# Performance work log

Hardware: AMD Instinct MI355X
Metric: run time of the kernel (lower is better)

Reference implementation:

```python
import jax, jax.numpy as jnp
import numpy as np

V, E, H, LM, LC = 50257, 512, 1024, 128, 256


def gru_cell(x, h, Wih, Whh, bih, bhh):
    # PyTorch nn.GRU cell, gate order (r, z, n)
    gi = x @ Wih.T + bih
    gh = h @ Whh.T + bhh
    i_r, i_z, i_n = jnp.split(gi, 3, -1)
    h_r, h_z, h_n = jnp.split(gh, 3, -1)
    r = jax.nn.sigmoid(i_r + h_r)
    z = jax.nn.sigmoid(i_z + h_z)
    n = jnp.tanh(i_n + r * h_n)
    return (1.0 - z) * n + z * h


def setup_inputs() -> dict:
    key = jax.random.key(0)
    ks = jax.random.split(key, 18)
    f = lambda k, sh: jax.random.normal(k, sh, jnp.float32) * 0.02
    return {
        "motion": jax.random.randint(ks[0], (1, LM), 0, V),
        "target_output": jax.random.randint(ks[1], (1, LC), 0, V),
        "enc_emb": f(ks[2], (V, E)),
        "enc_Wih": f(ks[3], (3 * H, E)),
        "enc_Whh": f(ks[4], (3 * H, H)),
        "enc_bih": f(ks[5], (3 * H,)),
        "enc_bhh": f(ks[6], (3 * H,)),
        "dec_emb": f(ks[7], (V, H)),
        "dec_Wih": f(ks[8], (3 * H, H)),
        "dec_Whh": f(ks[9], (3 * H, H)),
        "dec_bih": f(ks[10], (3 * H,)),
        "dec_bhh": f(ks[11], (3 * H,)),
        "attn_W": f(ks[12], (LM, 2 * H)),
        "attn_b": f(ks[13], (LM,)),
        "comb_W": f(ks[14], (H, 2 * H)),
        "comb_b": f(ks[15], (H,)),
        "out_W": f(ks[16], (V, H)),
        "out_b": f(ks[17], (V,)),
    }


def reference(motion, target_output, enc_emb, enc_Wih, enc_Whh, enc_bih, enc_bhh,
              dec_emb, dec_Wih, dec_Whh, dec_bih, dec_bhh,
              attn_W, attn_b, comb_W, comb_b, out_W, out_b):
    # ----- encode: per-step GRU over motion tokens (batch is hard-coded 1) -----
    toks = motion[0]  # [LM]

    def enc_step(h, t):
        h2 = gru_cell(enc_emb[t], h, enc_Wih, enc_Whh, enc_bih, enc_bhh)
        return h2, h2

    h0 = jnp.zeros((H,), jnp.float32)
    enc_h, enc_outs = jax.lax.scan(enc_step, h0, toks)  # enc_outs: [LM, H]

    # ----- decode with teacher forcing -----
    # original: decoder_input = SOS at idx 0, then target[idx-1] set at end of
    # step idx => step idx+1 consumes target[idx-1]; step 1 consumes target[-1].
    tgt = target_output[0]  # [LC]
    dec_in = jnp.concatenate([jnp.zeros((1,), tgt.dtype), tgt[-1:], tgt[:-2]])  # [LC]

    def dec_step(h, t):
        emb = dec_emb[t]  # [H] (dropout is identity at inference)
        attn_w = jax.nn.softmax(jnp.concatenate([emb, h]) @ attn_W.T + attn_b)  # [LM]
        ctx = attn_w @ enc_outs  # [H]
        x = jnp.concatenate([emb, ctx]) @ comb_W.T + comb_b  # [H] (no relu in source)
        h2 = gru_cell(x, h, dec_Wih, dec_Whh, dec_bih, dec_bhh)
        logp = jax.nn.log_softmax(h2 @ out_W.T + out_b)  # [V]
        return h2, logp

    _, logps = jax.lax.scan(dec_step, enc_h, dec_in)  # [LC, V]
    return logps[None]  # [1, LC, V] (permute(1,0,2) with batch=1)
```

## Files before the change

### kernel.cpp

```cpp
#include <hip/hip_runtime.h>

#define V_ 50257
#define E_ 512
#define H_ 1024
#define LM_ 128
#define LC_ 256
#define NBLK 256
#define ROWS 12
#define AREP 16

typedef __attribute__((ext_vector_type(8))) short short8;
typedef __attribute__((ext_vector_type(4))) float f32x4;
typedef unsigned long long u64;

__device__ __forceinline__ unsigned short f2bf(float x) {
  union { float f; unsigned u; } v; v.f = x;
  unsigned r = v.u + 0x7fffu + ((v.u >> 16) & 1u);
  return (unsigned short)(r >> 16);
}
__device__ __forceinline__ float bflo(unsigned u) { union { unsigned u; float f; } v; v.u = u << 16; return v.f; }
__device__ __forceinline__ float bfhi(unsigned u) { union { unsigned u; float f; } v; v.u = u & 0xffff0000u; return v.f; }

__device__ __forceinline__ int grow4(int s, int i0) {
  return (s < 4) ? (i0 + s) : (s < 8) ? (1024 + i0 + (s - 4)) : (2048 + i0 + (s - 8));
}

__device__ __forceinline__ void st_u32(unsigned* p, unsigned v) {
  __hip_atomic_store(p, v, __ATOMIC_RELAXED, __HIP_MEMORY_SCOPE_AGENT);
}
__device__ __forceinline__ void st_u64(u64* p, u64 v) {
  __hip_atomic_store(p, v, __ATOMIC_RELAXED, __HIP_MEMORY_SCOPE_AGENT);
}
__device__ __forceinline__ u64 ld_u64(const u64* p) {
  return __hip_atomic_load(p, __ATOMIC_RELAXED, __HIP_MEMORY_SCOPE_AGENT);
}
__device__ __forceinline__ unsigned ld_u32(const unsigned* p) {
  return __hip_atomic_load(p, __ATOMIC_RELAXED, __HIP_MEMORY_SCOPE_AGENT);
}
__device__ __forceinline__ float ld_f32(const float* p) {
  return __hip_atomic_load(p, __ATOMIC_RELAXED, __HIP_MEMORY_SCOPE_AGENT);
}
__device__ __forceinline__ void atom_add_f32(float* p, float v) {
  (void)__hip_atomic_fetch_add(p, v, __ATOMIC_RELAXED, __HIP_MEMORY_SCOPE_AGENT);
}

__global__ void gather_enc(const int* __restrict__ motion, const float* __restrict__ emb,
                           float* __restrict__ dst) {
  int t = blockIdx.x;
  int tok = motion[t];
  const float4* s = (const float4*)(emb + (size_t)tok * E_);
  float4* d = (float4*)(dst + (size_t)t * E_);
  d[threadIdx.x] = s[threadIdx.x];
}

__global__ void gather_dec(const int* __restrict__ tgt, const float* __restrict__ emb,
                           float* __restrict__ dst) {
  int t = blockIdx.x;
  int tok = (t == 0) ? 0 : (t == 1 ? tgt[LC_ - 1] : tgt[t - 2]);
  const float4* s = (const float4*)(emb + (size_t)tok * H_);
  float4* d = (float4*)(dst + (size_t)t * H_);
  d[threadIdx.x] = s[threadIdx.x];
}

__global__ __launch_bounds__(256) void gemm_f32(const float* __restrict__ A, int lda,
                                                const float* __restrict__ B, int ldb,
                                                const float* __restrict__ bias,
                                                float* __restrict__ C, int ldc, int K) {
  __shared__ float As[16][68];
  __shared__ float Bs[16][68];
  const int bm = blockIdx.y * 64, bn = blockIdx.x * 64;
  const int tid = threadIdx.x;
  const int tx = tid & 15, ty = tid >> 4;
  const int lm = tid & 63, lk = (tid >> 6) * 4;
  float acc[4][4] = {};
  for (int k0 = 0; k0 < K; k0 += 16) {
    float4 av = *(const float4*)&A[(size_t)(bm + lm) * lda + k0 + lk];
    float4 bv = *(const float4*)&B[(size_t)(bn + lm) * ldb + k0 + lk];
    As[lk + 0][lm] = av.x; As[lk + 1][lm] = av.y; As[lk + 2][lm] = av.z; As[lk + 3][lm] = av.w;
    Bs[lk + 0][lm] = bv.x; Bs[lk + 1][lm] = bv.y; Bs[lk + 2][lm] = bv.z; Bs[lk + 3][lm] = bv.w;
    __syncthreads();
#pragma unroll
    for (int kk = 0; kk < 16; ++kk) {
      float4 a4 = *(const float4*)&As[kk][ty * 4];
      float4 b4 = *(const float4*)&Bs[kk][tx * 4];
      acc[0][0] += a4.x * b4.x; acc[0][1] += a4.x * b4.y; acc[0][2] += a4.x * b4.z; acc[0][3] += a4.x * b4.w;
      acc[1][0] += a4.y * b4.x; acc[1][1] += a4.y * b4.y; acc[1][2] += a4.y * b4.z; acc[1][3] += a4.y * b4.w;
      acc[2][0] += a4.z * b4.x; acc[2][1] += a4.z * b4.y; acc[2][2] += a4.z * b4.z; acc[2][3] += a4.z * b4.w;
      acc[3][0] += a4.w * b4.x; acc[3][1] += a4.w * b4.y; acc[3][2] += a4.w * b4.z; acc[3][3] += a4.w * b4.w;
    }
    __syncthreads();
  }
#pragma unroll
  for (int i = 0; i < 4; ++i) {
#pragma unroll
    for (int j = 0; j < 4; ++j) {
      int gm = bm + ty * 4 + i, gn = bn + tx * 4 + j;
      float bv = bias ? bias[gn] : 0.f;
      C[(size_t)gm * ldc + gn] = acc[i][j] + bv;
    }
  }
}

__global__ __launch_bounds__(256) void enc_rnn(const float* __restrict__ Whh,
                                               const float* __restrict__ bhh,
                                               const float* __restrict__ gi,
                                               u64* __restrict__ epk,
                                               float* __restrict__ outs) {
  __shared__ unsigned short Whl[ROWS][1024];
  __shared__ unsigned h_sh[512];
  __shared__ float h_own[4];
  __shared__ float bh[ROWS];
  __shared__ float ghl[ROWS];
  const int b = blockIdx.x, tid = threadIdx.x;
  const int w = tid >> 6, l = tid & 63;
  const int i0 = b * 4;
  for (int idx = tid; idx < ROWS * 1024; idx += 256) {
    int s = idx >> 10, c = idx & 1023;
    Whl[s][c] = f2bf(Whh[(size_t)grow4(s, i0) * H_ + c]);
  }
  if (tid < ROWS) bh[tid] = bhh[grow4(tid, i0)];
  if (tid < 4) h_own[tid] = 0.f;
  __syncthreads();

  for (int t = 0; t < LM_; ++t) {
    float gr = 0.f, gz = 0.f, gn_ = 0.f;
    if (tid < 4) {
      const float* git = gi + (size_t)t * 3072;
      gr = git[i0 + tid]; gz = git[1024 + i0 + tid]; gn_ = git[2048 + i0 + tid];
    }
    if (t == 0) {
      h_sh[2 * tid] = 0u; h_sh[2 * tid + 1] = 0u;
    } else {
      const u64* pb = epk + (size_t)(t & 1) * 512 + 2 * tid;
      const unsigned g = (unsigned)t;
      u64 q0, q1;
      for (;;) {
        q0 = ld_u64(pb); q1 = ld_u64(pb + 1);
        if ((unsigned)(q0 >> 32) == g && (unsigned)(q1 >> 32) == g) break;
        __builtin_amdgcn_s_sleep(1);
      }
      h_sh[2 * tid] = (unsigned)q0;
      h_sh[2 * tid + 1] = (unsigned)q1;
    }
    __syncthreads();

    for (int s = w; s < ROWS; s += 4) {
      float acc = 0.f;
#pragma unroll
      for (int e = 0; e < 8; ++e) {
        unsigned u = *(const unsigned*)&Whl[s][2 * (e * 64 + l)];
        unsigned hv = h_sh[e * 64 + l];
        acc += bflo(u) * bflo(hv) + bfhi(u) * bfhi(hv);
      }
#pragma unroll
      for (int off = 32; off; off >>= 1) acc += __shfl_xor(acc, off);
      if (l == 0) ghl[s] = acc;
    }
    __syncthreads();
    if (tid < 4) {
      int i = tid, ig = i0 + i;
      float hr = ghl[i] + bh[i], hz = ghl[4 + i] + bh[4 + i], hn = ghl[8 + i] + bh[8 + i];
      float r = 1.f / (1.f + expf(-(gr + hr)));
      float z = 1.f / (1.f + expf(-(gz + hz)));
      float n = tanhf(gn_ + r * hn);
      float hpv = (1.f - z) * n + z * h_own[i];
      h_own[i] = hpv;
      float v0 = __shfl(hpv, 0), v1 = __shfl(hpv, 1);
      float v2 = __shfl(hpv, 2), v3 = __shfl(hpv, 3);
      if (tid == 0) {
        u64 gg = (u64)(unsigned)(t + 1) << 32;
        u64* pb = epk + (size_t)((t + 1) & 1) * 512 + 2 * b;
        st_u64(pb,     gg | (u64)((unsigned)f2bf(v0) | ((unsigned)f2bf(v1) << 16)));
        st_u64(pb + 1, gg | (u64)((unsigned)f2bf(v2) | ((unsigned)f2bf(v3) << 16)));
      }
      outs[(size_t)t * H_ + ig] = hpv;
    }
  }
}

__global__ __launch_bounds__(256) void dec_rnn(const float* __restrict__ Whh,
                                               const float* __restrict__ bhh,
                                               const float* __restrict__ attn_W,
                                               const float* __restrict__ G,
                                               const float* __restrict__ P1,
                                               const float* __restrict__ aE,
                                               const float* __restrict__ hfin,
                                               float* __restrict__ a_acc,
                                               u64* __restrict__ dpk,
                                               unsigned* __restrict__ dflags,
                                               unsigned short* __restrict__ Hs) {
  __shared__ unsigned short Whl[ROWS][1024];
  __shared__ unsigned Ac[2 * 128];
  __shared__ float Gl[ROWS][128];
  __shared__ unsigned h_sh[512];
  __shared__ float a_f[128];
  __shared__ float tmp2[256];
  __shared__ float h_own[4];
  __shared__ float bh[ROWS];
  __shared__ float ghl[ROWS];
  __shared__ float giS[ROWS];
  const int b = blockIdx.x, tid = threadIdx.x;
  const int w = tid >> 6, l = tid & 63;
  const int i0 = b * 4;
  for (int idx = tid; idx < ROWS * 1024; idx += 256) {
    int s = idx >> 10, c = idx & 1023;
    Whl[s][c] = f2bf(Whh[(size_t)grow4(s, i0) * H_ + c]);
  }
  if (tid < 256) {
    int u = tid >> 7, j = tid & 127;
    float2 wv = *(const float2*)&attn_W[(size_t)j * 2048 + 1024 + i0 + 2 * u];
    Ac[tid] = (unsigned)f2bf(wv.x) | ((unsigned)f2bf(wv.y) << 16);
  }
  for (int idx = tid; idx < ROWS * 128; idx += 256) {
    int s = idx >> 7, c = idx & 127;
    Gl[s][c] = G[(size_t)grow4(s, i0) * 128 + c];
  }
  if (tid < ROWS) bh[tid] = bhh[grow4(tid, i0)];
  if (tid < 4) h_own[tid] = hfin[i0 + tid];
  __syncthreads();

  {
    float h0 = h_own[0], h1 = h_own[1], h2 = h_own[2], h3 = h_own[3];
    if (tid < 128) {
      unsigned w0 = Ac[tid], w1 = Ac[128 + tid];
      float a0 = bflo(w0) * h0 + bfhi(w0) * h1 + bflo(w1) * h2 + bfhi(w1) * h3;
      atom_add_f32(&a_acc[(b & (AREP - 1)) * 128 + tid], a0);
    }
    __syncthreads();
    if (tid == 0) st_u32(&dflags[b * 16], 1u);
  }

  for (int t = 0; t < LC_; ++t) {
    float aEp = 0.f;
    if (tid < 128) aEp = aE[(size_t)t * LM_ + tid];
    float p1p[3];
    if (l == 0) {
#pragma unroll
      for (int k = 0; k < 3; ++k) p1p[k] = P1[(size_t)t * 3072 + grow4(w + 4 * k, i0)];
    } else {
      p1p[0] = p1p[1] = p1p[2] = 0.f;
    }

    if (t == 0) {
      float4 hv = ((const float4*)hfin)[tid];
      h_sh[2 * tid] = (unsigned)f2bf(hv.x) | ((unsigned)f2bf(hv.y) << 16);
      h_sh[2 * tid + 1] = (unsigned)f2bf(hv.z) | ((unsigned)f2bf(hv.w) << 16);
    } else {
      const u64* pb = dpk + (size_t)(t & 1) * 512 + 2 * tid;
      const unsigned g = (unsigned)t;
      u64 q0, q1;
      for (;;) {
        q0 = ld_u64(pb); q1 = ld_u64(pb + 1);
        if ((unsigned)(q0 >> 32) == g && (unsigned)(q1 >> 32) == g) break;
        __builtin_amdgcn_s_sleep(1);
      }
      h_sh[2 * tid] = (unsigned)q0;
      h_sh[2 * tid + 1] = (unsigned)q1;
    }
    __syncthreads();

    for (int s = w; s < ROWS; s += 4) {
      float acc = 0.f;
#pragma unroll
      for (int e = 0; e < 8; ++e) {
        unsigned u = *(const unsigned*)&Whl[s][2 * (e * 64 + l)];
        unsigned hv = h_sh[e * 64 + l];
        acc += bflo(u) * bflo(hv) + bfhi(u) * bfhi(hv);
      }
#pragma unroll
      for (int off = 32; off; off >>= 1) acc += __shfl_xor(acc, off);
      if (l == 0) ghl[s] = acc;
    }
    if (tid < 64) {
      const unsigned need = (unsigned)(t + 1);
      for (;;) {
        unsigned f0 = ld_u32(&dflags[tid * 16]);
        unsigned f1 = ld_u32(&dflags[(tid + 64) * 16]);
        unsigned f2 = ld_u32(&dflags[(tid + 128) * 16]);
        unsigned f3 = ld_u32(&dflags[(tid + 192) * 16]);
        unsigned mn = min(min(f0, f1), min(f2, f3));
        if (__all((int)(mn >= need))) break;
        __builtin_amdgcn_s_sleep(1);
      }
    }
    __syncthreads();
    {
      int j = tid & 127, half = tid >> 7;
      const float* ab = a_acc + (size_t)t * (AREP * 128) + half * 8 * 128 + j;
      float p = 0.f;
#pragma unroll
      for (int r = 0; r < 8; ++r) p += ld_f32(ab + r * 128);
      tmp2[tid] = p;
    }
    __syncthreads();
    if (tid < 128) a_f[tid] = tmp2[tid] + tmp2[tid + 128] + aEp;
    __syncthreads();

    float ax = a_f[2 * l], ay = a_f[2 * l + 1];
    float mx = fmaxf(ax, ay);
#pragma unroll
    for (int off = 32; off; off >>= 1) mx = fmaxf(mx, __shfl_xor(mx, off));
    float pe0 = expf(ax - mx), pe1 = expf(ay - mx);
    float zs = pe0 + pe1;
#pragma unroll
    for (int off = 32; off; off >>= 1) zs += __shfl_xor(zs, off);
    float w0 = pe0 / zs, w1 = pe1 / zs;
#pragma unroll
    for (int k = 0; k < 3; ++k) {
      int s = w + 4 * k;
      float2 g2 = *(const float2*)&Gl[s][2 * l];
      float acc = g2.x * w0 + g2.y * w1;
#pragma unroll
      for (int off = 32; off; off >>= 1) acc += __shfl_xor(acc, off);
      if (l == 0) giS[s] = acc + p1p[k];
    }
    __syncthreads();

    if (tid < 4) {
      int i = tid, ig = i0 + i;
      float hr = ghl[i] + bh[i], hz = ghl[4 + i] + bh[4 + i], hn = ghl[8 + i] + bh[8 + i];
      float r = 1.f / (1.f + expf(-(giS[i] + hr)));
      float z = 1.f / (1.f + expf(-(giS[4 + i] + hz)));
      float n = tanhf(giS[8 + i] + r * hn);
      float hpv = (1.f - z) * n + z * h_own[i];
      h_own[i] = hpv;
      float v0 = __shfl(hpv, 0), v1 = __shfl(hpv, 1);
      float v2 = __shfl(hpv, 2), v3 = __shfl(hpv, 3);
      if (tid == 0 && t < LC_ - 1) {
        u64 gg = (u64)(unsigned)(t + 1) << 32;
        u64* pb = dpk + (size_t)((t + 1) & 1) * 512 + 2 * b;
        st_u64(pb,     gg | (u64)((unsigned)f2bf(v0) | ((unsigned)f2bf(v1) << 16)));
        st_u64(pb + 1, gg | (u64)((unsigned)f2bf(v2) | ((unsigned)f2bf(v3) << 16)));
      }
      Hs[(size_t)t * H_ + ig] = f2bf(hpv);
    }
    __syncthreads();

    if (t < LC_ - 1) {
      float h0 = h_own[0], h1 = h_own[1], h2 = h_own[2], h3 = h_own[3];
      if (tid < 128) {
        unsigned w0p = Ac[tid], w1p = Ac[128 + tid];
        float a0 = bflo(w0p) * h0 + bfhi(w0p) * h1 + bflo(w1p) * h2 + bfhi(w1p) * h3;
        atom_add_f32(&a_acc[(size_t)(t + 1) * (AREP * 128) + (b & (AREP - 1)) * 128 + tid], a0);
      }
    }
    __syncthreads();
    if (tid == 0) st_u32(&dflags[b * 16], (unsigned)(t + 2));
  }
}

__global__ __launch_bounds__(256) void out_gemm(const unsigned short* __restrict__ A,
                                                const float* __restrict__ Wf, int ldw,
                                                const float* __restrict__ bias,
                                                float* __restrict__ C, int N, int K) {
  __shared__ unsigned short As[256][40];
  __shared__ unsigned short Bs[64][40];
  const int bn = blockIdx.x * 64;
  const int tid = threadIdx.x, w = tid >> 6, l = tid & 63;
  f32x4 acc[4][4];
#pragma unroll
  for (int mf = 0; mf < 4; ++mf)
#pragma unroll
    for (int nf = 0; nf < 4; ++nf) acc[mf][nf] = (f32x4){0.f, 0.f, 0.f, 0.f};

  for (int k0 = 0; k0 < K; k0 += 32) {
    const unsigned short* src = A + (size_t)tid * K + k0;
#pragma unroll
    for (int kc = 0; kc < 4; ++kc) {
      short8 v = *(const short8*)(src + kc * 8);
      *(short8*)&As[tid][kc * 8] = v;
    }
#pragma unroll
    for (int c = 0; c < 2; ++c) {
      int idx = tid + c * 256;
      int n = idx >> 3, kc = idx & 7;
      int gn = bn + n;
      float4 v = {0.f, 0.f, 0.f, 0.f};
      if (gn < N) v = *(const float4*)&Wf[(size_t)gn * ldw + k0 + kc * 4];
      uint2 p;
      p.x = (unsigned)f2bf(v.x) | ((unsigned)f2bf(v.y) << 16);
      p.y = (unsigned)f2bf(v.z) | ((unsigned)f2bf(v.w) << 16);
      *(uint2*)&Bs[n][kc * 4] = p;
    }
    __syncthreads();
    const int k8 = (l >> 4) * 8;
    short8 af4[4], bf4[4];
#pragma unroll
    for (int mf = 0; mf < 4; ++mf) af4[mf] = *(const short8*)&As[w * 64 + mf * 16 + (l & 15)][k8];
#pragma unroll
    for (int nf = 0; nf < 4; ++nf) bf4[nf] = *(const short8*)&Bs[nf * 16 + (l & 15)][k8];
#pragma unroll
    for (int mf = 0; mf < 4; ++mf)
#pragma unroll
      for (int nf = 0; nf < 4; ++nf)
        acc[mf][nf] = __builtin_amdgcn_mfma_f32_16x16x32_bf16(af4[mf], bf4[nf], acc[mf][nf], 0, 0, 0);
    __syncthreads();
  }
#pragma unroll
  for (int mf = 0; mf < 4; ++mf) {
#pragma unroll
    for (int nf = 0; nf < 4; ++nf) {
      int n = bn + nf * 16 + (l & 15);
      if (n < N) {
        float bv = bias[n];
#pragma unroll
        for (int i = 0; i < 4; ++i) {
          int m = w * 64 + mf * 16 + (l >> 4) * 4 + i;
          C[(size_t)m * N + n] = acc[mf][nf][i] + bv;
        }
      }
    }
  }
}

__global__ __launch_bounds__(256) void lsm_stats(const float* __restrict__ C, float* __restrict__ stats, int N) {
  const int r = blockIdx.x, tid = threadIdx.x, w = tid >> 6, l = tid & 63;
  __shared__ float red[4];
  const float* row = C + (size_t)r * N;
  float m = -3.4e38f;
  for (int i = tid; i < N; i += 256) m = fmaxf(m, row[i]);
#pragma unroll
  for (int off = 32; off; off >>= 1) m = fmaxf(m, __shfl_xor(m, off));
  if (l == 0) red[w] = m;
  __syncthreads();
  m = fmaxf(fmaxf(red[0], red[1]), fmaxf(red[2], red[3]));
  __syncthreads();
  float s = 0.f;
  for (int i = tid; i < N; i += 256) s += expf(row[i] - m);
#pragma unroll
  for (int off = 32; off; off >>= 1) s += __shfl_xor(s, off);
  if (l == 0) red[w] = s;
  __syncthreads();
  if (tid == 0) {
    stats[r] = m;
    stats[256 + r] = logf(red[0] + red[1] + red[2] + red[3]);
  }
}

__global__ __launch_bounds__(256) void lsm_apply(float* __restrict__ C, const float* __restrict__ stats, int N) {
  int r = blockIdx.y;
  int ci = blockIdx.x * 256 + threadIdx.x;
  if (ci < N) {
    size_t idx = (size_t)r * N + ci;
    C[idx] = C[idx] - stats[r] - stats[256 + r];
  }
}

extern "C" void kernel_launch(void* const* d_in, const int* in_sizes, int n_in,
                              void* d_out, int out_size, void* d_ws, size_t ws_size,
                              hipStream_t stream) {
  (void)in_sizes; (void)n_in; (void)out_size; (void)ws_size;
  const int* motion = (const int*)d_in[0];
  const int* tgt = (const int*)d_in[1];
  const float* enc_emb = (const float*)d_in[2];
  const float* enc_Wih = (const float*)d_in[3];
  const float* enc_Whh = (const float*)d_in[4];
  const float* enc_bih = (const float*)d_in[5];
  const float* enc_bhh = (const float*)d_in[6];
  const float* dec_emb = (const float*)d_in[7];
  const float* dec_Wih = (const float*)d_in[8];
  const float* dec_Whh = (const float*)d_in[9];
  const float* dec_bih = (const float*)d_in[10];
  const float* dec_bhh = (const float*)d_in[11];
  const float* attn_W = (const float*)d_in[12];
  const float* attn_b = (const float*)d_in[13];
  const float* comb_W = (const float*)d_in[14];
  const float* comb_b = (const float*)d_in[15];
  const float* out_W = (const float*)d_in[16];
  const float* out_b = (const float*)d_in[17];
  float* out = (float*)d_out;

  float* wsf = (float*)d_ws;
  size_t o = 0;
  auto F = [&](size_t n) { float* p = wsf + o; o += (n + 3) & ~(size_t)3; return p; };
  float* enc_gi = F(128 * 3072);
  float* enc_outs = F(128 * 1024);
  float* embA = F(128 * 512);
  float* demb = F(256 * 1024);
  float* aE = F(256 * 128);
  float* xE = F(256 * 1024);
  float* P1 = F(256 * 3072);
  float* M2T = F(128 * 1024);
  float* Gm = F(3072 * 128);
  u64* epk = (u64*)F(2048);
  u64* dpk = (u64*)F(2048);
  unsigned* dflags = (unsigned*)F(4096);
  float* a_acc = F(LC_ * AREP * 128);
  float* stats = F(512);
  unsigned short* Hs = (unsigned short*)F(256 * 1024 / 2);

  hipMemsetAsync(epk, 0, (2048 + 2048 + 4096 + LC_ * AREP * 128) * sizeof(float), stream);

  gather_enc<<<128, 128, 0, stream>>>(motion, enc_emb, embA);
  gemm_f32<<<dim3(48, 2), 256, 0, stream>>>(embA, 512, enc_Wih, 512, enc_bih, enc_gi, 3072, 512);
  gather_dec<<<256, 256, 0, stream>>>(tgt, dec_emb, demb);
  gemm_f32<<<dim3(2, 4), 256, 0, stream>>>(demb, 1024, attn_W, 2048, attn_b, aE, 128, 1024);
  gemm_f32<<<dim3(16, 4), 256, 0, stream>>>(demb, 1024, comb_W, 2048, comb_b, xE, 1024, 1024);
  gemm_f32<<<dim3(48, 4), 256, 0, stream>>>(xE, 1024, dec_Wih, 1024, dec_bih, P1, 3072, 1024);

  enc_rnn<<<NBLK, 256, 0, stream>>>(enc_Whh, enc_bhh, enc_gi, epk, enc_outs);

  gemm_f32<<<dim3(16, 2), 256, 0, stream>>>(enc_outs, 1024, comb_W + 1024, 2048, nullptr, M2T, 1024, 1024);
  gemm_f32<<<dim3(2, 48), 256, 0, stream>>>(dec_Wih, 1024, M2T, 1024, nullptr, Gm, 128, 1024);

  dec_rnn<<<NBLK, 256, 0, stream>>>(dec_Whh, dec_bhh, attn_W, Gm, P1, aE,
                                    enc_outs + (size_t)(LM_ - 1) * H_, a_acc, dpk, dflags, Hs);

  out_gemm<<<786, 256, 0, stream>>>(Hs, out_W, 1024, out_b, out, V_, 1024);
  lsm_stats<<<256, 256, 0, stream>>>(out, stats, V_);
  lsm_apply<<<dim3(197, 256), 256, 0, stream>>>(out, stats, V_);
}
```

Baseline: 2.505 ms.

## Fuse embedding gathers into GEMMs and compute log-softmax partials in output GEMM epilogue

Measured after the change: 2.384 ms. 4.8% less time.

```diff
diff --git a/kernel.cpp b/kernel.cpp
--- a/kernel.cpp
+++ b/kernel.cpp
@@ -8,6 +8,7 @@
 #define NBLK 256
 #define ROWS 12
 #define AREP 16
+#define NT_OUT 786
 
 typedef __attribute__((ext_vector_type(8))) short short8;
 typedef __attribute__((ext_vector_type(4))) float f32x4;
@@ -44,37 +45,27 @@
   (void)__hip_atomic_fetch_add(p, v, __ATOMIC_RELAXED, __HIP_MEMORY_SCOPE_AGENT);
 }
 
-__global__ void gather_enc(const int* __restrict__ motion, const float* __restrict__ emb,
-                           float* __restrict__ dst) {
-  int t = blockIdx.x;
-  int tok = motion[t];
-  const float4* s = (const float4*)(emb + (size_t)tok * E_);
-  float4* d = (float4*)(dst + (size_t)t * E_);
-  d[threadIdx.x] = s[threadIdx.x];
-}
-
-__global__ void gather_dec(const int* __restrict__ tgt, const float* __restrict__ emb,
-                           float* __restrict__ dst) {
-  int t = blockIdx.x;
-  int tok = (t == 0) ? 0 : (t == 1 ? tgt[LC_ - 1] : tgt[t - 2]);
-  const float4* s = (const float4*)(emb + (size_t)tok * H_);
-  float4* d = (float4*)(dst + (size_t)t * H_);
-  d[threadIdx.x] = s[threadIdx.x];
-}
-
-__global__ __launch_bounds__(256) void gemm_f32(const float* __restrict__ A, int lda,
-                                                const float* __restrict__ B, int ldb,
-                                                const float* __restrict__ bias,
-                                                float* __restrict__ C, int ldc, int K) {
+__global__ void build_dec_tok(const int* __restrict__ tgt, int* __restrict__ dtok) {
+  int t = threadIdx.x;
+  dtok[t] = (t == 0) ? 0 : (t == 1 ? tgt[LC_ - 1] : tgt[t - 2]);
+}
+
+__global__ __launch_bounds__(256) void gemm_g(const float* __restrict__ A, int lda,
+                                              const int* __restrict__ ridx,
+                                              const float* __restrict__ B, int ldb,
+                                              const float* __restrict__ bias,
+                                              float* __restrict__ C, int ldc, int K) {
   __shared__ float As[16][68];
   __shared__ float Bs[16][68];
   const int bm = blockIdx.y * 64, bn = blockIdx.x * 64;
   const int tid = threadIdx.x;
   const int tx = tid & 15, ty = tid >> 4;
   const int lm = tid & 63, lk = (tid >> 6) * 4;
+  const int arow = ridx ? ridx[bm + lm] : (bm + lm);
+  const float* Arow = A + (size_t)arow * lda;
   float acc[4][4] = {};
   for (int k0 = 0; k0 < K; k0 += 16) {
-    float4 av = *(const float4*)&A[(size_t)(bm + lm) * lda + k0 + lk];
+    float4 av = *(const float4*)&Arow[k0 + lk];
     float4 bv = *(const float4*)&B[(size_t)(bn + lm) * ldb + k0 + lk];
     As[lk + 0][lm] = av.x; As[lk + 1][lm] = av.y; As[lk + 2][lm] = av.z; As[lk + 3][lm] = av.w;
     Bs[lk + 0][lm] = bv.x; Bs[lk + 1][lm] = bv.y; Bs[lk + 2][lm] = bv.z; Bs[lk + 3][lm] = bv.w;
@@ -97,6 +88,57 @@
       int gm = bm + ty * 4 + i, gn = bn + tx * 4 + j;
       float bv = bias ? bias[gn] : 0.f;
       C[(size_t)gm * ldc + gn] = acc[i][j] + bv;
+    }
+  }
+}
+
+__global__ __launch_bounds__(256) void gemm_dual(const float* __restrict__ A, int lda,
+                                                 const int* __restrict__ ridx,
+                                                 const float* __restrict__ combW,
+                                                 const float* __restrict__ comb_b,
+                                                 const float* __restrict__ attnW,
+                                                 const float* __restrict__ attn_b,
+                                                 float* __restrict__ xE,
+                                                 float* __restrict__ aE, int K) {
+  __shared__ float As[16][68];
+  __shared__ float Bs[16][68];
+  const int bm = blockIdx.y * 64;
+  const bool is_x = blockIdx.x < 16;
+  const int bn = (is_x ? blockIdx.x : (blockIdx.x - 16)) * 64;
+  const float* B = is_x ? combW : attnW;
+  const int ldb = 2048;
+  const float* bias = is_x ? comb_b : attn_b;
+  float* C = is_x ? xE : aE;
+  const int ldc = is_x ? 1024 : 128;
+  const int tid = threadIdx.x;
+  const int tx = tid & 15, ty = tid >> 4;
+  const int lm = tid & 63, lk = (tid >> 6) * 4;
+  const int arow = ridx[bm + lm];
+  const float* Arow = A + (size_t)arow * lda;
+  float acc[4][4] = {};
+  for (int k0 = 0; k0 < K; k0 += 16) {
+    float4 av = *(const float4*)&Arow[k0 + lk];
+    float4 bv = *(const float4*)&B[(size_t)(bn + lm) * ldb + k0 + lk];
+    As[lk + 0][lm] = av.x; As[lk + 1][lm] = av.y; As[lk + 2][lm] = av.z; As[lk + 3][lm] = av.w;
+    Bs[lk + 0][lm] = bv.x; Bs[lk + 1][lm] = bv.y; Bs[lk + 2][lm] = bv.z; Bs[lk + 3][lm] = bv.w;
+    __syncthreads();
+#pragma unroll
+    for (int kk = 0; kk < 16; ++kk) {
+      float4 a4 = *(const float4*)&As[kk][ty * 4];
+      float4 b4 = *(const float4*)&Bs[kk][tx * 4];
+      acc[0][0] += a4.x * b4.x; acc[0][1] += a4.x * b4.y; acc[0][2] += a4.x * b4.z; acc[0][3] += a4.x * b4.w;
+      acc[1][0] += a4.y * b4.x; acc[1][1] += a4.y * b4.y; acc[1][2] += a4.y * b4.z; acc[1][3] += a4.y * b4.w;
+      acc[2][0] += a4.z * b4.x; acc[2][1] += a4.z * b4.y; acc[2][2] += a4.z * b4.z; acc[2][3] += a4.z * b4.w;
+      acc[3][0] += a4.w * b4.x; acc[3][1] += a4.w * b4.y; acc[3][2] += a4.w * b4.z; acc[3][3] += a4.w * b4.w;
+    }
+    __syncthreads();
+  }
+#pragma unroll
+  for (int i = 0; i < 4; ++i) {
+#pragma unroll
+    for (int j = 0; j < 4; ++j) {
+      int gm = bm + ty * 4 + i, gn = bn + tx * 4 + j;
+      C[(size_t)gm * ldc + gn] = acc[i][j] + bias[gn];
     }
   }
 }
@@ -352,10 +394,13 @@
 __global__ __launch_bounds__(256) void out_gemm(const unsigned short* __restrict__ A,
                                                 const float* __restrict__ Wf, int ldw,
                                                 const float* __restrict__ bias,
-                                                float* __restrict__ C, int N, int K) {
+                                                float* __restrict__ C,
+                                                float* __restrict__ pmax,
+                                                float* __restrict__ psum,
+                                                int N, int K) {
   __shared__ unsigned short As[256][40];
   __shared__ unsigned short Bs[64][40];
-  const int bn = blockIdx.x * 64;
+  const int bn = blockIdx.x * 64, bx = blockIdx.x;
   const int tid = threadIdx.x, w = tid >> 6, l = tid & 63;
   f32x4 acc[4][4];
 #pragma unroll
@@ -399,40 +444,60 @@
 #pragma unroll
   for (int mf = 0; mf < 4; ++mf) {
 #pragma unroll
-    for (int nf = 0; nf < 4; ++nf) {
-      int n = bn + nf * 16 + (l & 15);
-      if (n < N) {
-        float bv = bias[n];
-#pragma unroll
-        for (int i = 0; i < 4; ++i) {
-          int m = w * 64 + mf * 16 + (l >> 4) * 4 + i;
-          C[(size_t)m * N + n] = acc[mf][nf][i] + bv;
+    for (int i = 0; i < 4; ++i) {
+      int m = w * 64 + mf * 16 + (l >> 4) * 4 + i;
+      float v[4];
+#pragma unroll
+      for (int nf = 0; nf < 4; ++nf) {
+        int n = bn + nf * 16 + (l & 15);
+        float val = -3.4e38f;
+        if (n < N) {
+          val = acc[mf][nf][i] + bias[n];
+          C[(size_t)m * N + n] = val;
         }
-      }
-    }
-  }
-}
-
-__global__ __launch_bounds__(256) void lsm_stats(const float* __restrict__ C, float* __restrict__ stats, int N) {
+        v[nf] = val;
+      }
+      float mv = fmaxf(fmaxf(v[0], v[1]), fmaxf(v[2], v[3]));
+#pragma unroll
+      for (int off = 1; off < 16; off <<= 1) mv = fmaxf(mv, __shfl_xor(mv, off));
+      float se = 0.f;
+#pragma unroll
+      for (int nf = 0; nf < 4; ++nf) se += (v[nf] > -1e38f) ? expf(v[nf] - mv) : 0.f;
+#pragma unroll
+      for (int off = 1; off < 16; off <<= 1) se += __shfl_xor(se, off);
+      if ((l & 15) == 0) {
+        pmax[(size_t)m * NT_OUT + bx] = mv;
+        psum[(size_t)m * NT_OUT + bx] = se;
+      }
+    }
+  }
+}
+
+__global__ __launch_bounds__(256) void lsm_combine(const float* __restrict__ pmax,
+                                                   const float* __restrict__ psum,
+                                                   float* __restrict__ stats) {
   const int r = blockIdx.x, tid = threadIdx.x, w = tid >> 6, l = tid & 63;
   __shared__ float red[4];
-  const float* row = C + (size_t)r * N;
+  __shared__ float Msh;
+  const float* pm = pmax + (size_t)r * NT_OUT;
+  const float* ps = psum + (size_t)r * NT_OUT;
   float m = -3.4e38f;
-  for (int i = tid; i < N; i += 256) m = fmaxf(m, row[i]);
+  for (int j = tid; j < NT_OUT; j += 256) m = fmaxf(m, pm[j]);
 #pragma unroll
   for (int off = 32; off; off >>= 1) m = fmaxf(m, __shfl_xor(m, off));
   if (l == 0) red[w] = m;
   __syncthreads();
-  m = fmaxf(fmaxf(red[0], red[1]), fmaxf(red[2], red[3]));
+  if (tid == 0) Msh = fmaxf(fmaxf(red[0], red[1]), fmaxf(red[2], red[3]));
   __syncthreads();
+  float M = Msh;
   float s = 0.f;
-  for (int i = tid; i < N; i += 256) s += expf(row[i] - m);
+  for (int j = tid; j < NT_OUT; j += 256) s += ps[j] * expf(pm[j] - M);
 #pragma unroll
   for (int off = 32; off; off >>= 1) s += __shfl_xor(s, off);
   if (l == 0) red[w] = s;
   __syncthreads();
   if (tid == 0) {
-    stats[r] = m;
+    stats[r] = M;
     stats[256 + r] = logf(red[0] + red[1] + red[2] + red[3]);
   }
 }
@@ -475,38 +540,37 @@
   auto F = [&](size_t n) { float* p = wsf + o; o += (n + 3) & ~(size_t)3; return p; };
   float* enc_gi = F(128 * 3072);
   float* enc_outs = F(128 * 1024);
-  float* embA = F(128 * 512);
-  float* demb = F(256 * 1024);
   float* aE = F(256 * 128);
   float* xE = F(256 * 1024);
   float* P1 = F(256 * 3072);
   float* M2T = F(128 * 1024);
   float* Gm = F(3072 * 128);
+  int* dec_tok = (int*)F(256);
   u64* epk = (u64*)F(2048);
   u64* dpk = (u64*)F(2048);
   unsigned* dflags = (unsigned*)F(4096);
   float* a_acc = F(LC_ * AREP * 128);
   float* stats = F(512);
+  float* pmax = F(256 * NT_OUT);
+  float* psum = F(256 * NT_OUT);
   unsigned short* Hs = (unsigned short*)F(256 * 1024 / 2);
 
   hipMemsetAsync(epk, 0, (2048 + 2048 + 4096 + LC_ * AREP * 128) * sizeof(float), stream);
 
-  gather_enc<<<128, 128, 0, stream>>>(motion, enc_emb, embA);
-  gemm_f32<<<dim3(48, 2), 256, 0, stream>>>(embA, 512, enc_Wih, 512, enc_bih, enc_gi, 3072, 512);
-  gather_dec<<<256, 256, 0, stream>>>(tgt, dec_emb, demb);
-  gemm_f32<<<dim3(2, 4), 256, 0, stream>>>(demb, 1024, attn_W, 2048, attn_b, aE, 128, 1024);
-  gemm_f32<<<dim3(16, 4), 256, 0, stream>>>(demb, 1024, comb_W, 2048, comb_b, xE, 1024, 1024);
-  gemm_f32<<<dim3(48, 4), 256, 0, stream>>>(xE, 1024, dec_Wih, 1024, dec_bih, P1, 3072, 1024);
+  build_dec_tok<<<1, 256, 0, stream>>>(tgt, dec_tok);
+  gemm_g<<<dim3(48, 2), 256, 0, stream>>>(enc_emb, 512, motion, enc_Wih, 512, enc_bih, enc_gi, 3072, 512);
+  gemm_dual<<<dim3(18, 4), 256, 0, stream>>>(dec_emb, 1024, dec_tok, comb_W, comb_b, attn_W, attn_b, xE, aE, 1024);
+  gemm_g<<<dim3(48, 4), 256, 0, stream>>>(xE, 1024, nullptr, dec_Wih, 1024, dec_bih, P1, 3072, 1024);
 
   enc_rnn<<<NBLK, 256, 0, stream>>>(enc_Whh, enc_bhh, enc_gi, epk, enc_outs);
 
-  gemm_f32<<<dim3(16, 2), 256, 0, stream>>>(enc_outs, 1024, comb_W + 1024, 2048, nullptr, M2T, 1024, 1024);
-  gemm_f32<<<dim3(2, 48), 256, 0, stream>>>(dec_Wih, 1024, M2T, 1024, nullptr, Gm, 128, 1024);
+  gemm_g<<<dim3(16, 2), 256, 0, stream>>>(enc_outs, 1024, nullptr, comb_W + 1024, 2048, nullptr, M2T, 1024, 1024);
+  gemm_g<<<dim3(2, 48), 256, 0, stream>>>(dec_Wih, 1024, nullptr, M2T, 1024, nullptr, Gm, 128, 1024);
 
   dec_rnn<<<NBLK, 256, 0, stream>>>(dec_Whh, dec_bhh, attn_W, Gm, P1, aE,
                                     enc_outs + (size_t)(LM_ - 1) * H_, a_acc, dpk, dflags, Hs);
 
-  out_gemm<<<786, 256, 0, stream>>>(Hs, out_W, 1024, out_b, out, V_, 1024);
-  lsm_stats<<<256, 256, 0, stream>>>(out, stats, V_);
+  out_gemm<<<NT_OUT, 256, 0, stream>>>(Hs, out_W, 1024, out_b, out, pmax, psum, V_, 1024);
+  lsm_combine<<<256, 256, 0, stream>>>(pmax, psum, stats);
   lsm_apply<<<dim3(197, 256), 256, 0, stream>>>(out, stats, V_);
 }
```
